# Optimization experiments

Measured on AMD Instinct MI355X. Metric: run time of the kernel, lower is better.

## Reference

```python
import jax, jax.numpy as jnp
import numpy as np

EPS_CR = 0.5      # eps in coding rate
ETA = 0.5
LAMBDA_LAP = 0.3
LN_EPS = 1e-5


def setup_inputs() -> dict:
    key = jax.random.key(0)
    ks = jax.random.split(key, 8)
    n, in_dim, out_dim, d_sub, K1 = 8192, 256, 128, 64, 3
    H = jax.random.normal(ks[0], (n, in_dim), jnp.float32)
    hop_feats = jax.random.normal(ks[1], (K1, n, in_dim), jnp.float32)
    L = jax.random.normal(ks[2], (n, n), jnp.float32) * 0.01
    W_stack = jax.random.normal(ks[3], (K1, d_sub, in_dim), jnp.float32) * 0.05
    W_out = jax.random.normal(ks[4], (out_dim, in_dim), jnp.float32) * 0.05
    threshold = jnp.full((out_dim,), 0.05, jnp.float32)
    ln_gamma = jnp.ones((out_dim,), jnp.float32)
    ln_beta = jnp.zeros((out_dim,), jnp.float32)
    tau = jnp.asarray(1.0, jnp.float32)
    return {"H": H, "hop_feats": hop_feats, "L": L, "W_stack": W_stack,
            "W_out": W_out, "threshold": threshold, "ln_gamma": ln_gamma,
            "ln_beta": ln_beta, "tau": tau}


def reference(H, hop_feats, L, W_stack, W_out, threshold, ln_gamma, ln_beta, tau):
    n = H.shape[0]
    d = W_stack.shape[1]
    coeff = d / (n * EPS_CR * EPS_CR)
    # per-hop subspace projections: Z [K+1, n, d]
    Z = jnp.einsum('knf,kdf->knd', hop_feats, W_stack)
    # shared Gram M = I + coeff * Z^T Z  [K+1, d, d]
    G = jnp.einsum('knd,kne->kde', Z, Z)
    M = jnp.eye(d, dtype=Z.dtype)[None] + coeff * G
    # coding rates via batched slogdet
    _, logdet = jnp.linalg.slogdet(M)
    R = 0.5 * logdet                                    # [K+1]
    # delta_R: first entry is R[0], rest are successive diffs
    delta_R = R - jnp.concatenate([jnp.zeros((1,), R.dtype), R[:-1]])
    dR_norm = (delta_R - delta_R.mean()) / (jnp.std(delta_R, ddof=1) + 1e-6)
    w = jax.nn.softmax(dR_norm / tau)                   # [K+1]
    # coding-rate gradients: g_Z = coeff * Z @ M^{-1} via batched solve
    g_Z = coeff * jnp.linalg.solve(M, jnp.swapaxes(Z, 1, 2))  # [K+1, d, n]
    # g_H[k] = g_Z[k]^T @ W[k]; weighted sum over hops -> [n, in_dim]
    grad_contrib = jnp.einsum('k,kdn,kdf->nf', w, g_Z, W_stack)
    H_half = H + ETA * grad_contrib - ETA * LAMBDA_LAP * (L @ H)
    # in_dim != out_dim -> project
    H_pre = H_half @ W_out.T                            # [n, out_dim]
    thr = jnp.abs(threshold)[None, :]
    H_soft = jnp.sign(H_pre) * jnp.maximum(jnp.abs(H_pre) - thr, 0.0)
    # LayerNorm over last dim
    mu = H_soft.mean(-1, keepdims=True)
    var = jnp.mean((H_soft - mu) ** 2, -1, keepdims=True)
    H_out = (H_soft - mu) * jax.lax.rsqrt(var + LN_EPS) * ln_gamma + ln_beta
    return (H_out, w, jax.lax.stop_gradient(dR_norm), jax.lax.stop_gradient(delta_R))
```

## Files before the change

### kernel.cpp

```cpp
#include <hip/hip_runtime.h>
#include <hip/hip_bf16.h>
#include <math.h>


#define COEFF 0.03125f
#define SCL_LAP (-0.15f)

typedef __attribute__((ext_vector_type(8))) short short8;
typedef __attribute__((ext_vector_type(4))) float f32x4;

__device__ __forceinline__ unsigned short f2bf_bits(float f) {
  unsigned int u = __float_as_uint(f);
  unsigned int r = (u + 0x7fffu + ((u >> 16) & 1u)) >> 16;
  return (unsigned short)r;
}

__global__ __launch_bounds__(256) void gemm_tile(
    const float* __restrict__ A, const float* __restrict__ B,
    float* __restrict__ C, const float* __restrict__ addC,
    const float* __restrict__ scale_ptr,
    int K, int lda, int ldb, int ldc, int ldadd,
    long sA, long sB, long sC, int transB) {
  __shared__ __align__(16) float As[16][68];
  __shared__ __align__(16) float Bs[16][68];
  const int tid = threadIdx.x;
  const int tx = tid & 15, ty = tid >> 4;
  const int m0 = blockIdx.y * 64, n0 = blockIdx.x * 64;
  const int b = blockIdx.z;
  A += (size_t)b * sA; B += (size_t)b * sB; C += (size_t)b * sC;
  float cc[4][4];
#pragma unroll
  for (int i = 0; i < 4; ++i)
#pragma unroll
    for (int j = 0; j < 4; ++j) cc[i][j] = 0.f;
  const int lr = tid >> 2, lc = (tid & 3) << 2;
  for (int k0 = 0; k0 < K; k0 += 16) {
    float4 av = *(const float4*)(A + (size_t)(m0 + lr) * lda + k0 + lc);
    As[lc][lr] = av.x; As[lc + 1][lr] = av.y; As[lc + 2][lr] = av.z; As[lc + 3][lr] = av.w;
    if (transB) {
      float4 bv = *(const float4*)(B + (size_t)(n0 + lr) * ldb + k0 + lc);
      Bs[lc][lr] = bv.x; Bs[lc + 1][lr] = bv.y; Bs[lc + 2][lr] = bv.z; Bs[lc + 3][lr] = bv.w;
    } else {
      int kk = tid & 15, n4 = (tid >> 4) << 2;
      float4 bv = *(const float4*)(B + (size_t)(k0 + kk) * ldb + n0 + n4);
      *(float4*)&Bs[kk][n4] = bv;
    }
    __syncthreads();
#pragma unroll
    for (int kk = 0; kk < 16; ++kk) {
      float4 a4 = *(const float4*)&As[kk][ty * 4];
      float4 b4 = *(const float4*)&Bs[kk][tx * 4];
      float a[4] = {a4.x, a4.y, a4.z, a4.w};
      float bb[4] = {b4.x, b4.y, b4.z, b4.w};
#pragma unroll
      for (int i = 0; i < 4; ++i)
#pragma unroll
        for (int j = 0; j < 4; ++j) cc[i][j] = fmaf(a[i], bb[j], cc[i][j]);
    }
    __syncthreads();
  }
  float scale = scale_ptr ? scale_ptr[b] : 1.0f;
#pragma unroll
  for (int i = 0; i < 4; ++i)
#pragma unroll
    for (int j = 0; j < 4; ++j) {
      int m = m0 + ty * 4 + i, n = n0 + tx * 4 + j;
      float v = cc[i][j] * scale;
      if (addC) v += addC[(size_t)m * ldadd + n];
      C[(size_t)m * ldc + n] = v;
    }
}

__global__ __launch_bounds__(256) void gram_kernel(const float* __restrict__ Z,
                                                   float* __restrict__ Gpart) {
  __shared__ __align__(16) float Zs[64][68];
  const int k = blockIdx.y, tid = threadIdx.x;
  const int d0 = (tid & 15) * 4, e0 = (tid >> 4) * 4;
  float acc[4][4];
#pragma unroll
  for (int i = 0; i < 4; ++i)
#pragma unroll
    for (int j = 0; j < 4; ++j) acc[i][j] = 0.f;
  for (int c = 0; c < 4; ++c) {
    int nb = blockIdx.x * 256 + c * 64;
    for (int idx = tid; idx < 1024; idx += 256) {
      int rr = idx >> 4, c4 = (idx & 15) * 4;
      float4 v = *(const float4*)(Z + (size_t)(nb + rr) * 192 + k * 64 + c4);
      *(float4*)&Zs[rr][c4] = v;
    }
    __syncthreads();
    for (int rr = 0; rr < 64; ++rr) {
      float4 zd4 = *(const float4*)&Zs[rr][d0];
      float4 ze4 = *(const float4*)&Zs[rr][e0];
      float zd[4] = {zd4.x, zd4.y, zd4.z, zd4.w};
      float ze[4] = {ze4.x, ze4.y, ze4.z, ze4.w};
#pragma unroll
      for (int i = 0; i < 4; ++i)
#pragma unroll
        for (int j = 0; j < 4; ++j) acc[i][j] = fmaf(zd[i], ze[j], acc[i][j]);
    }
    __syncthreads();
  }
  float* g = Gpart + (size_t)(k * 32 + blockIdx.x) * 4096;
#pragma unroll
  for (int i = 0; i < 4; ++i)
#pragma unroll
    for (int j = 0; j < 4; ++j) g[(d0 + i) * 64 + (e0 + j)] = acc[i][j];
}

__device__ __forceinline__ float blocksum256(float v, volatile float* scr) {
#pragma unroll
  for (int o = 32; o; o >>= 1) v += __shfl_xor(v, o);
  __syncthreads();
  if ((threadIdx.x & 63) == 0) scr[threadIdx.x >> 6] = v;
  __syncthreads();
  return scr[0] + scr[1] + scr[2] + scr[3];
}

__device__ __forceinline__ void gemm64s(const float* X, const float* Y,
                                        float acc[4][4]) {
  const int tx = threadIdx.x & 15, ty = threadIdx.x >> 4;
#pragma unroll
  for (int i = 0; i < 4; ++i)
#pragma unroll
    for (int j = 0; j < 4; ++j) acc[i][j] = 0.f;
  for (int kk = 0; kk < 64; ++kk) {
    float4 a4 = *(const float4*)&X[kk * 64 + ty * 4];
    float4 b4 = *(const float4*)&Y[kk * 64 + tx * 4];
    float a[4] = {a4.x, a4.y, a4.z, a4.w};
    float bb[4] = {b4.x, b4.y, b4.z, b4.w};
#pragma unroll
    for (int i = 0; i < 4; ++i)
#pragma unroll
      for (int j = 0; j < 4; ++j) acc[i][j] = fmaf(a[i], bb[j], acc[i][j]);
  }
}

__device__ __forceinline__ void wb64(float* D, const float acc[4][4]) {
  const int tx = threadIdx.x & 15, ty = threadIdx.x >> 4;
#pragma unroll
  for (int i = 0; i < 4; ++i)
#pragma unroll
    for (int j = 0; j < 4; ++j) D[(ty * 4 + i) * 64 + tx * 4 + j] = acc[i][j];
}

__device__ __forceinline__ float dot64(const float* X, const float* Y, float* scr) {
  const int tx = threadIdx.x & 15, ty = threadIdx.x >> 4;
  float v = 0.f;
#pragma unroll
  for (int i = 0; i < 4; ++i)
#pragma unroll
    for (int j = 0; j < 4; ++j) {
      int idx = (ty * 4 + i) * 64 + tx * 4 + j;
      v += X[idx] * Y[idx];
    }
  return blocksum256(v, scr);
}

__global__ __launch_bounds__(256) void fused_big(
    const float* __restrict__ Lp, const unsigned short* __restrict__ HpT,
    float* __restrict__ Pbuf, const float* __restrict__ Gpart,
    float* __restrict__ Minv, float* __restrict__ Rout) {
  __shared__ __align__(16) float smem[12304];
  const int tid = threadIdx.x;

  if (blockIdx.x >= 3) {
    unsigned short (*As)[40] = (unsigned short(*)[40])smem;
    unsigned short (*Bs)[40] = (unsigned short(*)[40])(smem + 2560);
    const int g = blockIdx.x - 3;
    const int m0 = (g & 63) * 128;
    const int split = g >> 6;
    const int kbase = split * 1024;
    const int wave = tid >> 6, lane = tid & 63;
    const int ar = tid >> 1, ah = (tid & 1) * 16;
    const size_t lrow = (size_t)(m0 + ar) * 8192;
    const size_t brow = (size_t)ar * 8192;
    f32x4 acc[2][8];
#pragma unroll
    for (int i = 0; i < 2; ++i)
#pragma unroll
      for (int j = 0; j < 8; ++j) acc[i][j] = (f32x4){0.f, 0.f, 0.f, 0.f};
    float4 apf[4];
    uint4 bpf[2];
    {
      const float* ap = Lp + lrow + kbase + ah;
      apf[0] = *(const float4*)(ap); apf[1] = *(const float4*)(ap + 4);
      apf[2] = *(const float4*)(ap + 8); apf[3] = *(const float4*)(ap + 12);
      const unsigned short* bp = HpT + brow + kbase + ah;
      bpf[0] = *(const uint4*)(bp); bpf[1] = *(const uint4*)(bp + 8);
    }
    const int quad = lane >> 4, mcol = lane & 15;
    for (int step = 0; step < 32; ++step) {
      __syncthreads();
      {
        __attribute__((aligned(16))) unsigned short tmp[16];
        const float* f = (const float*)apf;
#pragma unroll
        for (int i = 0; i < 16; ++i) tmp[i] = f2bf_bits(f[i]);
        *(uint4*)&As[ar][ah] = *(const uint4*)&tmp[0];
        *(uint4*)&As[ar][ah + 8] = *(const uint4*)&tmp[8];
        *(uint4*)&Bs[ar][ah] = bpf[0];
        *(uint4*)&Bs[ar][ah + 8] = bpf[1];
      }
      __syncthreads();
      if (step < 31) {
        int kc = kbase + (step + 1) * 32;
        const float* ap = Lp + lrow + kc + ah;
        apf[0] = *(const float4*)(ap); apf[1] = *(const float4*)(ap + 4);
        apf[2] = *(const float4*)(ap + 8); apf[3] = *(const float4*)(ap + 12);
        const unsigned short* bp = HpT + brow + kc + ah;
        bpf[0] = *(const uint4*)(bp); bpf[1] = *(const uint4*)(bp + 8);
      }
      short8 af0 = *(const short8*)&As[wave * 32 + mcol][quad * 8];
      short8 af1 = *(const short8*)&As[wave * 32 + 16 + mcol][quad * 8];
#pragma unroll
      for (int nt = 0; nt < 8; ++nt) {
        short8 bf = *(const short8*)&Bs[nt * 16 + mcol][quad * 8];
        acc[0][nt] = __builtin_amdgcn_mfma_f32_16x16x32_bf16(af0, bf, acc[0][nt], 0, 0, 0);
        acc[1][nt] = __builtin_amdgcn_mfma_f32_16x16x32_bf16(af1, bf, acc[1][nt], 0, 0, 0);
      }
    }
    float* P = Pbuf + (size_t)split * 1048576;
#pragma unroll
    for (int mt = 0; mt < 2; ++mt)
#pragma unroll
      for (int nt = 0; nt < 8; ++nt)
#pragma unroll
        for (int r = 0; r < 4; ++r) {
          int grow = m0 + wave * 32 + mt * 16 + quad * 4 + r;
          int gcol = nt * 16 + mcol;
          P[(size_t)grow * 128 + gcol] = acc[mt][nt][r];
        }
    return;
  }

  const int k = blockIdx.x;
  float* B0 = smem;
  float* B1 = smem + 4096;
  float* B2 = smem + 8192;
  float* scr = smem + 12288;
  for (int i = tid; i < 4096; i += 256) {
    float s = 0.f;
    const float* gp = Gpart + (size_t)k * 32 * 4096 + i;
    for (int b = 0; b < 32; ++b) s += gp[b * 4096];
    B0[i] = COEFF * s + ((i >> 6) == (i & 63) ? 1.f : 0.f);
  }
  __syncthreads();
  if (tid < 64) {
    float rs = 0.f, dg = B0[tid * 65];
    for (int j = 0; j < 64; ++j) rs += fabsf(B0[j * 64 + tid]);
    float lo = 2.f * dg - rs, hi = rs;
#pragma unroll
    for (int o = 32; o; o >>= 1) {
      lo = fminf(lo, __shfl_xor(lo, o));
      hi = fmaxf(hi, __shfl_xor(hi, o));
    }
    if (tid == 0) scr[4] = 0.5f * (fmaxf(lo, 1.f) + hi);
  }
  __syncthreads();
  const float alpha = scr[4], inva = 1.f / alpha;
  for (int i = tid; i < 4096; i += 256) {
    int r = i >> 6, c = i & 63;
    B0[i] = B0[i] * inva - (r == c ? 1.f : 0.f);
  }
  __syncthreads();
  const int tx = tid & 15, ty = tid >> 4;
  float v1 = 0.f, v2 = 0.f;
#pragma unroll
  for (int i = 0; i < 4; ++i)
#pragma unroll
    for (int j = 0; j < 4; ++j) {
      int r = ty * 4 + i, c = tx * 4 + j;
      float e = B0[r * 64 + c];
      if (r == c) v1 += e;
      v2 += e * e;
    }
  float t1 = blocksum256(v1, scr);
  float t2 = blocksum256(v2, scr);
  float acc[4][4];
  gemm64s(B0, B0, acc); __syncthreads(); wb64(B1, acc); __syncthreads();
  float t3 = dot64(B1, B0, scr);
  float t4 = dot64(B1, B1, scr);
  gemm64s(B1, B0, acc); __syncthreads(); wb64(B2, acc); __syncthreads();
  float t5 = dot64(B2, B1, scr);
  float t6 = dot64(B2, B2, scr);
  gemm64s(B1, B1, acc);
  {
    float v7 = 0.f, v8 = 0.f;
#pragma unroll
    for (int i = 0; i < 4; ++i)
#pragma unroll
      for (int j = 0; j < 4; ++j) {
        int idx = (ty * 4 + i) * 64 + tx * 4 + j;
        v7 += acc[i][j] * B2[idx];
        v8 += acc[i][j] * acc[i][j];
      }
    float t7 = blocksum256(v7, scr);
    float t8 = blocksum256(v8, scr);
    if (tid == 0) {
      float ld = 64.f * logf(alpha) + t1 - t2 * 0.5f + t3 / 3.f - t4 * 0.25f
                 + t5 * 0.2f - t6 / 6.f + t7 / 7.f - t8 * 0.125f;
      Rout[k] = 0.5f * ld;
    }
  }
  for (int i = tid; i < 4096; i += 256) {
    int r = i >> 6, c = i & 63;
    B1[i] = (r == c ? 1.f : 0.f) - B0[i];
  }
  __syncthreads();
  for (int it = 0; it < 2; ++it) {
    gemm64s(B0, B1, acc);
    __syncthreads();
    {
#pragma unroll
      for (int i = 0; i < 4; ++i)
#pragma unroll
        for (int j = 0; j < 4; ++j) {
          int idx = (ty * 4 + i) * 64 + tx * 4 + j;
          B2[idx] = acc[i][j] + B1[idx];
        }
    }
    __syncthreads();
    gemm64s(B1, B2, acc);
    __syncthreads();
    {
#pragma unroll
      for (int i = 0; i < 4; ++i)
#pragma unroll
        for (int j = 0; j < 4; ++j) {
          int idx = (ty * 4 + i) * 64 + tx * 4 + j;
          B1[idx] = 2.f * B1[idx] - acc[i][j];
        }
    }
    __syncthreads();
  }
  for (int i = tid; i < 4096; i += 256) Minv[k * 4096 + i] = B1[i] * inva;
}

__global__ void small_w(const float* __restrict__ R, const float* __restrict__ tauP,
                        float* __restrict__ tail, float* __restrict__ sb) {
  if (threadIdx.x != 0) return;
  float R0 = R[0], R1 = R[1], R2 = R[2];
  float d0 = R0, d1 = R1 - R0, d2 = R2 - R1;
  float mean = (d0 + d1 + d2) * (1.f / 3.f);
  float e0 = d0 - mean, e1 = d1 - mean, e2 = d2 - mean;
  float sd = sqrtf((e0 * e0 + e1 * e1 + e2 * e2) * 0.5f) + 1e-6f;
  float n0 = e0 / sd, n1 = e1 / sd, n2 = e2 / sd;
  float tau = tauP[0];
  float x0 = n0 / tau, x1 = n1 / tau, x2 = n2 / tau;
  float mx = fmaxf(x0, fmaxf(x1, x2));
  float w0 = expf(x0 - mx), w1 = expf(x1 - mx), w2 = expf(x2 - mx);
  float s = w0 + w1 + w2;
  w0 /= s; w1 /= s; w2 /= s;
  tail[0] = w0; tail[1] = w1; tail[2] = w2;
  tail[3] = n0; tail[4] = n1; tail[5] = n2;
  tail[6] = d0; tail[7] = d1; tail[8] = d2;
  sb[0] = 0.015625f * w0; sb[1] = 0.015625f * w1; sb[2] = 0.015625f * w2;
}

__global__ __launch_bounds__(256) void transpose_cvt(const float* __restrict__ Hp,
                                                     unsigned short* __restrict__ HpT) {
  __shared__ float T[32][33];
  const int cb = blockIdx.x, rb = blockIdx.y, tid = threadIdx.x;
  int r = tid >> 3, c4 = (tid & 7) * 4;
  float4 v = *(const float4*)(Hp + (size_t)(rb * 32 + r) * 128 + cb * 32 + c4);
  T[r][c4] = v.x; T[r][c4 + 1] = v.y; T[r][c4 + 2] = v.z; T[r][c4 + 3] = v.w;
  __syncthreads();
  int c = tid >> 3, r4 = (tid & 7) * 4;
  ushort4 u;
  u.x = f2bf_bits(T[r4][c]); u.y = f2bf_bits(T[r4 + 1][c]);
  u.z = f2bf_bits(T[r4 + 2][c]); u.w = f2bf_bits(T[r4 + 3][c]);
  *(ushort4*)(HpT + (size_t)(cb * 32 + c) * 8192 + rb * 32 + r4) = u;
}

__global__ __launch_bounds__(256) void finish_kernel(
    const float* __restrict__ pre, const float* __restrict__ Pbuf,
    const float* __restrict__ thr, const float* __restrict__ gamma,
    const float* __restrict__ beta, float* __restrict__ out) {
  const int lane = threadIdx.x & 63;
  const int row = blockIdx.x * 4 + (threadIdx.x >> 6);
  const size_t off = (size_t)row * 128;
  float l0 = 0.f, l1 = 0.f;
#pragma unroll
  for (int s = 0; s < 8; ++s) {
    l0 += Pbuf[s * 1048576 + off + lane];
    l1 += Pbuf[s * 1048576 + off + lane + 64];
  }
  float x0 = pre[off + lane] + SCL_LAP * l0;
  float x1 = pre[off + lane + 64] + SCL_LAP * l1;
  float t0 = fabsf(thr[lane]), t1 = fabsf(thr[lane + 64]);
  float a0 = fmaxf(fabsf(x0) - t0, 0.f); float s0 = (x0 >= 0.f) ? a0 : -a0;
  float a1 = fmaxf(fabsf(x1) - t1, 0.f); float s1 = (x1 >= 0.f) ? a1 : -a1;
  float sum = s0 + s1;
#pragma unroll
  for (int o = 32; o; o >>= 1) sum += __shfl_xor(sum, o);
  float mean = sum * (1.f / 128.f);
  float d0 = s0 - mean, d1 = s1 - mean;
  float ss = d0 * d0 + d1 * d1;
#pragma unroll
  for (int o = 32; o; o >>= 1) ss += __shfl_xor(ss, o);
  float inv = rsqrtf(ss * (1.f / 128.f) + 1e-5f);
  out[off + lane] = d0 * inv * gamma[lane] + beta[lane];
  out[off + lane + 64] = d1 * inv * gamma[lane + 64] + beta[lane + 64];
}

extern "C" void kernel_launch(void* const* d_in, const int* in_sizes, int n_in,
                              void* d_out, int out_size, void* d_ws, size_t ws_size,
                              hipStream_t stream) {
  const float* H = (const float*)d_in[0];
  const float* hop = (const float*)d_in[1];
  const float* L = (const float*)d_in[2];
  const float* Wst = (const float*)d_in[3];
  const float* Wout = (const float*)d_in[4];
  const float* thr = (const float*)d_in[5];
  const float* gamma = (const float*)d_in[6];
  const float* beta = (const float*)d_in[7];
  const float* tau = (const float*)d_in[8];
  float* out = (float*)d_out;

  float* ws = (float*)d_ws;
  float* Zbuf = ws;
  float* Hp = Zbuf + 1572864;
  float* pre = Hp + 1048576;
  float* Gpart = pre + 1048576;
  float* Minv = Gpart + 393216;
  float* Rb = Minv + 12288;
  float* sb = Rb + 16;
  float* Pb = sb + 16;
  float* QT = Pb + 24576;
  float* Pbuf = QT + 24576;
  unsigned short* HpT = (unsigned short*)(Pbuf + 8388608);

  gemm_tile<<<dim3(2, 128, 1), 256, 0, stream>>>(
      H, Wout, Hp, nullptr, nullptr, 256, 256, 256, 128, 0, 0L, 0L, 0L, 1);
  transpose_cvt<<<dim3(4, 256), 256, 0, stream>>>(Hp, HpT);
  gemm_tile<<<dim3(1, 128, 3), 256, 0, stream>>>(
      hop, Wst, Zbuf, nullptr, nullptr, 256, 256, 256, 192, 0,
      2097152L, 16384L, 64L, 1);
  gram_kernel<<<dim3(32, 3), 256, 0, stream>>>(Zbuf, Gpart);
  gemm_tile<<<dim3(1, 2, 3), 256, 0, stream>>>(
      Wout, Wst, Pb, nullptr, nullptr, 256, 256, 256, 64, 0,
      0L, 16384L, 8192L, 1);
  fused_big<<<dim3(515), 256, 0, stream>>>(L, HpT, Pbuf, Gpart, Minv, Rb);
  small_w<<<dim3(1), 64, 0, stream>>>(Rb, tau, out + 1048576, sb);
  gemm_tile<<<dim3(1, 2, 3), 256, 0, stream>>>(
      Pb, Minv, QT, nullptr, sb, 64, 64, 64, 192, 0,
      8192L, 4096L, 64L, 0);
  gemm_tile<<<dim3(2, 128, 1), 256, 0, stream>>>(
      Zbuf, QT, pre, Hp, nullptr, 192, 192, 192, 128, 128, 0L, 0L, 0L, 1);
  finish_kernel<<<dim3(2048), 256, 0, stream>>>(pre, Pbuf, thr, gamma, beta, out);

  (void)in_sizes; (void)n_in; (void)out_size; (void)ws_size;
}
```

Measured before the change: 558.4 us.

## Fuse front GEMMs, transpose and Gram into one kernel; fuse back GEMM with LayerNorm

The separate GEMM, transpose, Gram and Pb launches become one multi-role front kernel. It computes per-tile Gram partials from Z held in registers and writes the bf16 transposed Hp straight from the tile. A new gsum kernel reduces the 128 Gram partials, and small_w is merged into the QT GEMM kernel. The final Z·Q GEMM is fused with the Laplacian partial sum, soft-threshold and LayerNorm, which removes the `pre` round trip and several launches. The cost is a larger Gram-partial buffer and an extra reduction launch.

Result: faster. 493.1 us (-11.7%).

```diff
diff --git a/kernel.cpp b/kernel.cpp
--- a/kernel.cpp
+++ b/kernel.cpp
@@ -15,20 +15,12 @@
   return (unsigned short)r;
 }
 
-__global__ __launch_bounds__(256) void gemm_tile(
+__device__ __forceinline__ void gemm_body(
     const float* __restrict__ A, const float* __restrict__ B,
-    float* __restrict__ C, const float* __restrict__ addC,
-    const float* __restrict__ scale_ptr,
-    int K, int lda, int ldb, int ldc, int ldadd,
-    long sA, long sB, long sC, int transB) {
-  __shared__ __align__(16) float As[16][68];
-  __shared__ __align__(16) float Bs[16][68];
+    int K, int lda, int ldb, int m0, int n0,
+    float* As, float* Bs, float cc[4][4]) {
   const int tid = threadIdx.x;
   const int tx = tid & 15, ty = tid >> 4;
-  const int m0 = blockIdx.y * 64, n0 = blockIdx.x * 64;
-  const int b = blockIdx.z;
-  A += (size_t)b * sA; B += (size_t)b * sB; C += (size_t)b * sC;
-  float cc[4][4];
 #pragma unroll
   for (int i = 0; i < 4; ++i)
 #pragma unroll
@@ -36,20 +28,16 @@
   const int lr = tid >> 2, lc = (tid & 3) << 2;
   for (int k0 = 0; k0 < K; k0 += 16) {
     float4 av = *(const float4*)(A + (size_t)(m0 + lr) * lda + k0 + lc);
-    As[lc][lr] = av.x; As[lc + 1][lr] = av.y; As[lc + 2][lr] = av.z; As[lc + 3][lr] = av.w;
-    if (transB) {
-      float4 bv = *(const float4*)(B + (size_t)(n0 + lr) * ldb + k0 + lc);
-      Bs[lc][lr] = bv.x; Bs[lc + 1][lr] = bv.y; Bs[lc + 2][lr] = bv.z; Bs[lc + 3][lr] = bv.w;
-    } else {
-      int kk = tid & 15, n4 = (tid >> 4) << 2;
-      float4 bv = *(const float4*)(B + (size_t)(k0 + kk) * ldb + n0 + n4);
-      *(float4*)&Bs[kk][n4] = bv;
-    }
+    As[(lc) * 68 + lr] = av.x; As[(lc + 1) * 68 + lr] = av.y;
+    As[(lc + 2) * 68 + lr] = av.z; As[(lc + 3) * 68 + lr] = av.w;
+    float4 bv = *(const float4*)(B + (size_t)(n0 + lr) * ldb + k0 + lc);
+    Bs[(lc) * 68 + lr] = bv.x; Bs[(lc + 1) * 68 + lr] = bv.y;
+    Bs[(lc + 2) * 68 + lr] = bv.z; Bs[(lc + 3) * 68 + lr] = bv.w;
     __syncthreads();
 #pragma unroll
     for (int kk = 0; kk < 16; ++kk) {
-      float4 a4 = *(const float4*)&As[kk][ty * 4];
-      float4 b4 = *(const float4*)&Bs[kk][tx * 4];
+      float4 a4 = *(const float4*)&As[kk * 68 + ty * 4];
+      float4 b4 = *(const float4*)&Bs[kk * 68 + tx * 4];
       float a[4] = {a4.x, a4.y, a4.z, a4.w};
       float bb[4] = {b4.x, b4.y, b4.z, b4.w};
 #pragma unroll
@@ -59,53 +47,109 @@
     }
     __syncthreads();
   }
-  float scale = scale_ptr ? scale_ptr[b] : 1.0f;
-#pragma unroll
-  for (int i = 0; i < 4; ++i)
-#pragma unroll
-    for (int j = 0; j < 4; ++j) {
-      int m = m0 + ty * 4 + i, n = n0 + tx * 4 + j;
-      float v = cc[i][j] * scale;
-      if (addC) v += addC[(size_t)m * ldadd + n];
-      C[(size_t)m * ldc + n] = v;
-    }
-}
-
-__global__ __launch_bounds__(256) void gram_kernel(const float* __restrict__ Z,
-                                                   float* __restrict__ Gpart) {
-  __shared__ __align__(16) float Zs[64][68];
-  const int k = blockIdx.y, tid = threadIdx.x;
-  const int d0 = (tid & 15) * 4, e0 = (tid >> 4) * 4;
-  float acc[4][4];
-#pragma unroll
-  for (int i = 0; i < 4; ++i)
-#pragma unroll
-    for (int j = 0; j < 4; ++j) acc[i][j] = 0.f;
-  for (int c = 0; c < 4; ++c) {
-    int nb = blockIdx.x * 256 + c * 64;
-    for (int idx = tid; idx < 1024; idx += 256) {
-      int rr = idx >> 4, c4 = (idx & 15) * 4;
-      float4 v = *(const float4*)(Z + (size_t)(nb + rr) * 192 + k * 64 + c4);
-      *(float4*)&Zs[rr][c4] = v;
-    }
-    __syncthreads();
-    for (int rr = 0; rr < 64; ++rr) {
-      float4 zd4 = *(const float4*)&Zs[rr][d0];
-      float4 ze4 = *(const float4*)&Zs[rr][e0];
+}
+
+__global__ __launch_bounds__(256) void front_kernel(
+    const float* __restrict__ H, const float* __restrict__ hop,
+    const float* __restrict__ Wst, const float* __restrict__ Wout,
+    float* __restrict__ Hp, unsigned short* __restrict__ HpT,
+    float* __restrict__ Zbuf, float* __restrict__ Gpart,
+    float* __restrict__ Pb) {
+  __shared__ __align__(16) float smem[4420];
+  float* As = smem;
+  float* Bs = smem + 1088;
+  const int tid = threadIdx.x;
+  const int tx = tid & 15, ty = tid >> 4;
+  float cc[4][4];
+  const int b = blockIdx.x;
+
+  if (b < 256) {
+    const int m0 = (b >> 1) * 64, n0 = (b & 1) * 64;
+    gemm_body(H, Wout, 256, 256, 256, m0, n0, As, Bs, cc);
+#pragma unroll
+    for (int i = 0; i < 4; ++i) {
+      float4 v = {cc[i][0], cc[i][1], cc[i][2], cc[i][3]};
+      *(float4*)(Hp + (size_t)(m0 + ty * 4 + i) * 128 + n0 + tx * 4) = v;
+    }
+#pragma unroll
+    for (int i = 0; i < 4; ++i)
+#pragma unroll
+      for (int j = 0; j < 4; ++j)
+        smem[(ty * 4 + i) * 65 + tx * 4 + j] = cc[i][j];
+    __syncthreads();
+    const int c = tid >> 2, mb = (tid & 3) << 4;
+    __attribute__((aligned(16))) unsigned short tmp[16];
+#pragma unroll
+    for (int t = 0; t < 16; ++t) tmp[t] = f2bf_bits(smem[(mb + t) * 65 + c]);
+    unsigned short* dst = HpT + (size_t)(n0 + c) * 8192 + m0 + mb;
+    *(uint4*)dst = *(const uint4*)&tmp[0];
+    *(uint4*)(dst + 8) = *(const uint4*)&tmp[8];
+  } else if (b < 640) {
+    const int i2 = b - 256;
+    const int k = i2 >> 7, mblk = i2 & 127;
+    const int m0 = mblk * 64;
+    gemm_body(hop + (size_t)k * 2097152, Wst + (size_t)k * 16384,
+              256, 256, 256, m0, 0, As, Bs, cc);
+#pragma unroll
+    for (int i = 0; i < 4; ++i) {
+      float4 v = {cc[i][0], cc[i][1], cc[i][2], cc[i][3]};
+      *(float4*)(Zbuf + (size_t)(m0 + ty * 4 + i) * 192 + k * 64 + tx * 4) = v;
+    }
+#pragma unroll
+    for (int i = 0; i < 4; ++i)
+#pragma unroll
+      for (int j = 0; j < 4; ++j)
+        smem[(ty * 4 + i) * 68 + tx * 4 + j] = cc[i][j];
+    __syncthreads();
+    float g[4][4];
+#pragma unroll
+    for (int i = 0; i < 4; ++i)
+#pragma unroll
+      for (int j = 0; j < 4; ++j) g[i][j] = 0.f;
+    const int d0 = tx * 4, e0 = ty * 4;
+    for (int r = 0; r < 64; ++r) {
+      float4 zd4 = *(const float4*)&smem[r * 68 + d0];
+      float4 ze4 = *(const float4*)&smem[r * 68 + e0];
       float zd[4] = {zd4.x, zd4.y, zd4.z, zd4.w};
       float ze[4] = {ze4.x, ze4.y, ze4.z, ze4.w};
 #pragma unroll
       for (int i = 0; i < 4; ++i)
 #pragma unroll
-        for (int j = 0; j < 4; ++j) acc[i][j] = fmaf(zd[i], ze[j], acc[i][j]);
-    }
-    __syncthreads();
-  }
-  float* g = Gpart + (size_t)(k * 32 + blockIdx.x) * 4096;
-#pragma unroll
-  for (int i = 0; i < 4; ++i)
-#pragma unroll
-    for (int j = 0; j < 4; ++j) g[(d0 + i) * 64 + (e0 + j)] = acc[i][j];
+        for (int j = 0; j < 4; ++j) g[i][j] = fmaf(zd[i], ze[j], g[i][j]);
+    }
+    float* gp = Gpart + ((size_t)k * 128 + mblk) * 4096;
+#pragma unroll
+    for (int i = 0; i < 4; ++i) {
+      float4 v = {g[i][0], g[i][1], g[i][2], g[i][3]};
+      *(float4*)(gp + (d0 + i) * 64 + e0) = v;
+    }
+  } else {
+    const int i2 = b - 640;
+    const int k = i2 >> 1;
+    const int m0 = (i2 & 1) * 64;
+    gemm_body(Wout, Wst + (size_t)k * 16384, 256, 256, 256, m0, 0, As, Bs, cc);
+    float* P = Pb + (size_t)k * 8192;
+#pragma unroll
+    for (int i = 0; i < 4; ++i) {
+      float4 v = {cc[i][0], cc[i][1], cc[i][2], cc[i][3]};
+      *(float4*)(P + (size_t)(m0 + ty * 4 + i) * 64 + tx * 4) = v;
+    }
+  }
+}
+
+__global__ __launch_bounds__(256) void gsum_kernel(
+    const float* __restrict__ Gpart, float* __restrict__ Gsum) {
+  const int k = blockIdx.x >> 4;
+  const int i = ((blockIdx.x & 15) << 8) + threadIdx.x;
+  const float* gp = Gpart + (size_t)k * 128 * 4096 + i;
+  float s0 = 0.f, s1 = 0.f, s2 = 0.f, s3 = 0.f;
+  for (int bb = 0; bb < 128; bb += 4) {
+    s0 += gp[(size_t)bb * 4096];
+    s1 += gp[(size_t)(bb + 1) * 4096];
+    s2 += gp[(size_t)(bb + 2) * 4096];
+    s3 += gp[(size_t)(bb + 3) * 4096];
+  }
+  Gsum[(size_t)k * 4096 + i] = (s0 + s1) + (s2 + s3);
 }
 
 __device__ __forceinline__ float blocksum256(float v, volatile float* scr) {
@@ -159,7 +203,7 @@
 
 __global__ __launch_bounds__(256) void fused_big(
     const float* __restrict__ Lp, const unsigned short* __restrict__ HpT,
-    float* __restrict__ Pbuf, const float* __restrict__ Gpart,
+    float* __restrict__ Pbuf, const float* __restrict__ Gsum,
     float* __restrict__ Minv, float* __restrict__ Rout) {
   __shared__ __align__(16) float smem[12304];
   const int tid = threadIdx.x;
@@ -240,10 +284,7 @@
   float* B2 = smem + 8192;
   float* scr = smem + 12288;
   for (int i = tid; i < 4096; i += 256) {
-    float s = 0.f;
-    const float* gp = Gpart + (size_t)k * 32 * 4096 + i;
-    for (int b = 0; b < 32; ++b) s += gp[b * 4096];
-    B0[i] = COEFF * s + ((i >> 6) == (i & 63) ? 1.f : 0.f);
+    B0[i] = COEFF * Gsum[(size_t)k * 4096 + i] + ((i >> 6) == (i & 63) ? 1.f : 0.f);
   }
   __syncthreads();
   if (tid < 64) {
@@ -337,71 +378,169 @@
   for (int i = tid; i < 4096; i += 256) Minv[k * 4096 + i] = B1[i] * inva;
 }
 
-__global__ void small_w(const float* __restrict__ R, const float* __restrict__ tauP,
-                        float* __restrict__ tail, float* __restrict__ sb) {
-  if (threadIdx.x != 0) return;
-  float R0 = R[0], R1 = R[1], R2 = R[2];
-  float d0 = R0, d1 = R1 - R0, d2 = R2 - R1;
-  float mean = (d0 + d1 + d2) * (1.f / 3.f);
-  float e0 = d0 - mean, e1 = d1 - mean, e2 = d2 - mean;
-  float sd = sqrtf((e0 * e0 + e1 * e1 + e2 * e2) * 0.5f) + 1e-6f;
-  float n0 = e0 / sd, n1 = e1 / sd, n2 = e2 / sd;
-  float tau = tauP[0];
-  float x0 = n0 / tau, x1 = n1 / tau, x2 = n2 / tau;
-  float mx = fmaxf(x0, fmaxf(x1, x2));
-  float w0 = expf(x0 - mx), w1 = expf(x1 - mx), w2 = expf(x2 - mx);
-  float s = w0 + w1 + w2;
-  w0 /= s; w1 /= s; w2 /= s;
-  tail[0] = w0; tail[1] = w1; tail[2] = w2;
-  tail[3] = n0; tail[4] = n1; tail[5] = n2;
-  tail[6] = d0; tail[7] = d1; tail[8] = d2;
-  sb[0] = 0.015625f * w0; sb[1] = 0.015625f * w1; sb[2] = 0.015625f * w2;
-}
-
-__global__ __launch_bounds__(256) void transpose_cvt(const float* __restrict__ Hp,
-                                                     unsigned short* __restrict__ HpT) {
-  __shared__ float T[32][33];
-  const int cb = blockIdx.x, rb = blockIdx.y, tid = threadIdx.x;
-  int r = tid >> 3, c4 = (tid & 7) * 4;
-  float4 v = *(const float4*)(Hp + (size_t)(rb * 32 + r) * 128 + cb * 32 + c4);
-  T[r][c4] = v.x; T[r][c4 + 1] = v.y; T[r][c4 + 2] = v.z; T[r][c4 + 3] = v.w;
-  __syncthreads();
-  int c = tid >> 3, r4 = (tid & 7) * 4;
-  ushort4 u;
-  u.x = f2bf_bits(T[r4][c]); u.y = f2bf_bits(T[r4 + 1][c]);
-  u.z = f2bf_bits(T[r4 + 2][c]); u.w = f2bf_bits(T[r4 + 3][c]);
-  *(ushort4*)(HpT + (size_t)(cb * 32 + c) * 8192 + rb * 32 + r4) = u;
-}
-
-__global__ __launch_bounds__(256) void finish_kernel(
-    const float* __restrict__ pre, const float* __restrict__ Pbuf,
+__global__ __launch_bounds__(256) void qtw_kernel(
+    const float* __restrict__ Pb, const float* __restrict__ Minv,
+    const float* __restrict__ R, const float* __restrict__ tauP,
+    float* __restrict__ QT, float* __restrict__ tail) {
+  __shared__ __align__(16) float XT[4096];
+  __shared__ __align__(16) float Y[4096];
+  __shared__ float wsh;
+  const int tid = threadIdx.x;
+  const int k = blockIdx.x >> 1;
+  const int m0 = (blockIdx.x & 1) * 64;
+  if (tid == 0) {
+    float R0 = R[0], R1 = R[1], R2 = R[2];
+    float d0 = R0, d1 = R1 - R0, d2 = R2 - R1;
+    float mean = (d0 + d1 + d2) * (1.f / 3.f);
+    float e0 = d0 - mean, e1 = d1 - mean, e2 = d2 - mean;
+    float sd = sqrtf((e0 * e0 + e1 * e1 + e2 * e2) * 0.5f) + 1e-6f;
+    float n0 = e0 / sd, n1 = e1 / sd, n2 = e2 / sd;
+    float tau = tauP[0];
+    float x0 = n0 / tau, x1 = n1 / tau, x2 = n2 / tau;
+    float mx = fmaxf(x0, fmaxf(x1, x2));
+    float w0 = expf(x0 - mx), w1 = expf(x1 - mx), w2 = expf(x2 - mx);
+    float s = w0 + w1 + w2;
+    w0 /= s; w1 /= s; w2 /= s;
+    wsh = 0.015625f * (k == 0 ? w0 : (k == 1 ? w1 : w2));
+    if (blockIdx.x == 0) {
+      tail[0] = w0; tail[1] = w1; tail[2] = w2;
+      tail[3] = n0; tail[4] = n1; tail[5] = n2;
+      tail[6] = d0; tail[7] = d1; tail[8] = d2;
+    }
+  }
+  {
+    const int m = tid >> 2, c4 = (tid & 3) << 4;
+    const float* src = Pb + (size_t)k * 8192 + (size_t)(m0 + m) * 64 + c4;
+#pragma unroll
+    for (int t = 0; t < 16; t += 4) {
+      float4 v = *(const float4*)(src + t);
+      XT[(c4 + t) * 64 + m] = v.x;
+      XT[(c4 + t + 1) * 64 + m] = v.y;
+      XT[(c4 + t + 2) * 64 + m] = v.z;
+      XT[(c4 + t + 3) * 64 + m] = v.w;
+    }
+    for (int t = tid * 4; t < 4096; t += 1024)
+      *(float4*)&Y[t] = *(const float4*)(Minv + (size_t)k * 4096 + t);
+  }
+  __syncthreads();
+  float acc[4][4];
+  gemm64s(XT, Y, acc);
+  const float s = wsh;
+  const int tx = tid & 15, ty = tid >> 4;
+#pragma unroll
+  for (int i = 0; i < 4; ++i) {
+    float4 v = {s * acc[i][0], s * acc[i][1], s * acc[i][2], s * acc[i][3]};
+    *(float4*)(QT + (size_t)(m0 + ty * 4 + i) * 192 + k * 64 + tx * 4) = v;
+  }
+}
+
+__global__ __launch_bounds__(256) void back_kernel(
+    const float* __restrict__ Zbuf, const float* __restrict__ QT,
+    const float* __restrict__ Hp, const float* __restrict__ Pbuf,
     const float* __restrict__ thr, const float* __restrict__ gamma,
     const float* __restrict__ beta, float* __restrict__ out) {
-  const int lane = threadIdx.x & 63;
-  const int row = blockIdx.x * 4 + (threadIdx.x >> 6);
-  const size_t off = (size_t)row * 128;
-  float l0 = 0.f, l1 = 0.f;
-#pragma unroll
-  for (int s = 0; s < 8; ++s) {
-    l0 += Pbuf[s * 1048576 + off + lane];
-    l1 += Pbuf[s * 1048576 + off + lane + 64];
-  }
-  float x0 = pre[off + lane] + SCL_LAP * l0;
-  float x1 = pre[off + lane + 64] + SCL_LAP * l1;
-  float t0 = fabsf(thr[lane]), t1 = fabsf(thr[lane + 64]);
-  float a0 = fmaxf(fabsf(x0) - t0, 0.f); float s0 = (x0 >= 0.f) ? a0 : -a0;
-  float a1 = fmaxf(fabsf(x1) - t1, 0.f); float s1 = (x1 >= 0.f) ? a1 : -a1;
-  float sum = s0 + s1;
-#pragma unroll
-  for (int o = 32; o; o >>= 1) sum += __shfl_xor(sum, o);
-  float mean = sum * (1.f / 128.f);
-  float d0 = s0 - mean, d1 = s1 - mean;
-  float ss = d0 * d0 + d1 * d1;
-#pragma unroll
-  for (int o = 32; o; o >>= 1) ss += __shfl_xor(ss, o);
-  float inv = rsqrtf(ss * (1.f / 128.f) + 1e-5f);
-  out[off + lane] = d0 * inv * gamma[lane] + beta[lane];
-  out[off + lane + 64] = d1 * inv * gamma[lane + 64] + beta[lane + 64];
+  __shared__ __align__(16) float As[16][36];
+  __shared__ __align__(16) float Bs[16][132];
+  const int tid = threadIdx.x;
+  const int tx = tid & 15, ty = tid >> 4;
+  const int m0 = blockIdx.x * 32;
+  float cc[2][8];
+#pragma unroll
+  for (int i = 0; i < 2; ++i)
+#pragma unroll
+    for (int j = 0; j < 8; ++j) cc[i][j] = 0.f;
+  const int lr = tid >> 2, lc = (tid & 3) << 2;
+  const int jr = tid >> 1, jc = (tid & 1) << 3;
+  for (int k0 = 0; k0 < 192; k0 += 16) {
+    if (tid < 128) {
+      float4 av = *(const float4*)(Zbuf + (size_t)(m0 + lr) * 192 + k0 + lc);
+      As[lc][lr] = av.x; As[lc + 1][lr] = av.y;
+      As[lc + 2][lr] = av.z; As[lc + 3][lr] = av.w;
+    }
+    {
+      const float* q = QT + (size_t)jr * 192 + k0 + jc;
+      float4 b0 = *(const float4*)(q);
+      float4 b1 = *(const float4*)(q + 4);
+      Bs[jc][jr] = b0.x; Bs[jc + 1][jr] = b0.y;
+      Bs[jc + 2][jr] = b0.z; Bs[jc + 3][jr] = b0.w;
+      Bs[jc + 4][jr] = b1.x; Bs[jc + 5][jr] = b1.y;
+      Bs[jc + 6][jr] = b1.z; Bs[jc + 7][jr] = b1.w;
+    }
+    __syncthreads();
+#pragma unroll
+    for (int kk = 0; kk < 16; ++kk) {
+      float2 a2 = *(const float2*)&As[kk][ty * 2];
+      float4 b4a = *(const float4*)&Bs[kk][tx * 8];
+      float4 b4b = *(const float4*)&Bs[kk][tx * 8 + 4];
+      float bb[8] = {b4a.x, b4a.y, b4a.z, b4a.w, b4b.x, b4b.y, b4b.z, b4b.w};
+#pragma unroll
+      for (int j = 0; j < 8; ++j) {
+        cc[0][j] = fmaf(a2.x, bb[j], cc[0][j]);
+        cc[1][j] = fmaf(a2.y, bb[j], cc[1][j]);
+      }
+    }
+    __syncthreads();
+  }
+  const float4 tA = *(const float4*)(thr + tx * 8);
+  const float4 tB = *(const float4*)(thr + tx * 8 + 4);
+  const float tv[8] = {fabsf(tA.x), fabsf(tA.y), fabsf(tA.z), fabsf(tA.w),
+                       fabsf(tB.x), fabsf(tB.y), fabsf(tB.z), fabsf(tB.w)};
+  const float4 gA = *(const float4*)(gamma + tx * 8);
+  const float4 gB = *(const float4*)(gamma + tx * 8 + 4);
+  const float gv[8] = {gA.x, gA.y, gA.z, gA.w, gB.x, gB.y, gB.z, gB.w};
+  const float4 bA = *(const float4*)(beta + tx * 8);
+  const float4 bB = *(const float4*)(beta + tx * 8 + 4);
+  const float bv[8] = {bA.x, bA.y, bA.z, bA.w, bB.x, bB.y, bB.z, bB.w};
+  float sres[2][8], mean[2], inv[2];
+#pragma unroll
+  for (int i = 0; i < 2; ++i) {
+    const size_t off = (size_t)(m0 + ty * 2 + i) * 128 + tx * 8;
+    float4 h0 = *(const float4*)(Hp + off);
+    float4 h1 = *(const float4*)(Hp + off + 4);
+    float p[8] = {0.f, 0.f, 0.f, 0.f, 0.f, 0.f, 0.f, 0.f};
+#pragma unroll
+    for (int sp = 0; sp < 8; ++sp) {
+      const float* pb = Pbuf + (size_t)sp * 1048576 + off;
+      float4 q0 = *(const float4*)(pb);
+      float4 q1 = *(const float4*)(pb + 4);
+      p[0] += q0.x; p[1] += q0.y; p[2] += q0.z; p[3] += q0.w;
+      p[4] += q1.x; p[5] += q1.y; p[6] += q1.z; p[7] += q1.w;
+    }
+    const float hv[8] = {h0.x, h0.y, h0.z, h0.w, h1.x, h1.y, h1.z, h1.w};
+    float sum = 0.f;
+#pragma unroll
+    for (int j = 0; j < 8; ++j) {
+      float x = cc[i][j] + hv[j] + SCL_LAP * p[j];
+      float a = fmaxf(fabsf(x) - tv[j], 0.f);
+      float sx = (x >= 0.f) ? a : -a;
+      sres[i][j] = sx;
+      sum += sx;
+    }
+#pragma unroll
+    for (int o = 1; o < 16; o <<= 1) sum += __shfl_xor(sum, o);
+    mean[i] = sum * (1.f / 128.f);
+    float ss = 0.f;
+#pragma unroll
+    for (int j = 0; j < 8; ++j) {
+      float dd = sres[i][j] - mean[i];
+      ss += dd * dd;
+    }
+#pragma unroll
+    for (int o = 1; o < 16; o <<= 1) ss += __shfl_xor(ss, o);
+    inv[i] = rsqrtf(ss * (1.f / 128.f) + 1e-5f);
+  }
+#pragma unroll
+  for (int i = 0; i < 2; ++i) {
+    const size_t off = (size_t)(m0 + ty * 2 + i) * 128 + tx * 8;
+    float o8[8];
+#pragma unroll
+    for (int j = 0; j < 8; ++j)
+      o8[j] = (sres[i][j] - mean[i]) * inv[i] * gv[j] + bv[j];
+    float4 v0 = {o8[0], o8[1], o8[2], o8[3]};
+    float4 v1 = {o8[4], o8[5], o8[6], o8[7]};
+    *(float4*)(out + off) = v0;
+    *(float4*)(out + off + 4) = v1;
+  }
 }
 
 extern "C" void kernel_launch(void* const* d_in, const int* in_sizes, int n_in,
@@ -421,34 +560,22 @@
   float* ws = (float*)d_ws;
   float* Zbuf = ws;
   float* Hp = Zbuf + 1572864;
-  float* pre = Hp + 1048576;
-  float* Gpart = pre + 1048576;
-  float* Minv = Gpart + 393216;
+  float* Gpart = Hp + 1048576;
+  float* Gsum = Gpart + 1572864;
+  float* Minv = Gsum + 12288;
   float* Rb = Minv + 12288;
-  float* sb = Rb + 16;
-  float* Pb = sb + 16;
+  float* Pb = Rb + 16;
   float* QT = Pb + 24576;
   float* Pbuf = QT + 24576;
   unsigned short* HpT = (unsigned short*)(Pbuf + 8388608);
 
-  gemm_tile<<<dim3(2, 128, 1), 256, 0, stream>>>(
-      H, Wout, Hp, nullptr, nullptr, 256, 256, 256, 128, 0, 0L, 0L, 0L, 1);
-  transpose_cvt<<<dim3(4, 256), 256, 0, stream>>>(Hp, HpT);
-  gemm_tile<<<dim3(1, 128, 3), 256, 0, stream>>>(
-      hop, Wst, Zbuf, nullptr, nullptr, 256, 256, 256, 192, 0,
-      2097152L, 16384L, 64L, 1);
-  gram_kernel<<<dim3(32, 3), 256, 0, stream>>>(Zbuf, Gpart);
-  gemm_tile<<<dim3(1, 2, 3), 256, 0, stream>>>(
-      Wout, Wst, Pb, nullptr, nullptr, 256, 256, 256, 64, 0,
-      0L, 16384L, 8192L, 1);
-  fused_big<<<dim3(515), 256, 0, stream>>>(L, HpT, Pbuf, Gpart, Minv, Rb);
-  small_w<<<dim3(1), 64, 0, stream>>>(Rb, tau, out + 1048576, sb);
-  gemm_tile<<<dim3(1, 2, 3), 256, 0, stream>>>(
-      Pb, Minv, QT, nullptr, sb, 64, 64, 64, 192, 0,
-      8192L, 4096L, 64L, 0);
-  gemm_tile<<<dim3(2, 128, 1), 256, 0, stream>>>(
-      Zbuf, QT, pre, Hp, nullptr, 192, 192, 192, 128, 128, 0L, 0L, 0L, 1);
-  finish_kernel<<<dim3(2048), 256, 0, stream>>>(pre, Pbuf, thr, gamma, beta, out);
+  front_kernel<<<dim3(646), 256, 0, stream>>>(H, hop, Wst, Wout,
+                                              Hp, HpT, Zbuf, Gpart, Pb);
+  gsum_kernel<<<dim3(48), 256, 0, stream>>>(Gpart, Gsum);
+  fused_big<<<dim3(515), 256, 0, stream>>>(L, HpT, Pbuf, Gsum, Minv, Rb);
+  qtw_kernel<<<dim3(6), 256, 0, stream>>>(Pb, Minv, Rb, tau, QT, out + 1048576);
+  back_kernel<<<dim3(256), 256, 0, stream>>>(Zbuf, QT, Hp, Pbuf,
+                                             thr, gamma, beta, out);
 
   (void)in_sizes; (void)n_in; (void)out_size; (void)ws_size;
 }
```
